# Optimization experiments

Measured on AMD Instinct MI355X. Metric: run time of the kernel, lower is better.

## Reference

```python
import jax, jax.numpy as jnp
import numpy as np


def conv1d(x, w, b, pad):
    # x: [B, C, T], w: [O, I, K], b: [O]
    y = jax.lax.conv_general_dilated(x, w, (1,), [(pad, pad)],
                                     dimension_numbers=('NCH', 'OIH', 'NCH'))
    return y + b[None, :, None]


def chan_ln(x, g, b, eps=1e-4):
    # channel LayerNorm on [B, C, T] (normalize over C)
    mu = jnp.mean(x, axis=1, keepdims=True)
    var = jnp.mean((x - mu) ** 2, axis=1, keepdims=True)
    return (x - mu) * jax.lax.rsqrt(var + eps) * g[None, :, None] + b[None, :, None]


def setup_inputs() -> dict:
    key = jax.random.key(0)
    ks = jax.random.split(key, 16)
    B, Tph, Tmel, H, W = 8, 512, 4096, 256, 256
    x = jax.random.normal(ks[0], (B, Tph, H), jnp.float32)
    x_mask = jnp.ones((B, Tph, 1), jnp.float32)
    x2word = jnp.sort(jax.random.randint(ks[1], (B, Tph), 1, W + 1), axis=1)
    mel2word = jnp.sort(jax.random.randint(ks[2], (B, Tmel), 1, W + 1), axis=1)
    s = 0.05
    pre_w1 = jax.random.normal(ks[3], (H, H, 5), jnp.float32) * s
    pre_b1 = jnp.zeros((H,), jnp.float32)
    ln1_g = jnp.ones((H,), jnp.float32)
    ln1_b = jnp.zeros((H,), jnp.float32)
    pre_w2 = jax.random.normal(ks[4], (H, H, 5), jnp.float32) * s
    pre_b2 = jnp.zeros((H,), jnp.float32)
    ln2_g = jnp.ones((H,), jnp.float32)
    ln2_b = jnp.zeros((H,), jnp.float32)
    proj_w = jax.random.normal(ks[5], (H, H, 1), jnp.float32) * s
    proj_b = jnp.zeros((H,), jnp.float32)
    gauss_w = jax.random.normal(ks[6], (2, H, 1), jnp.float32) * s
    gauss_b = jnp.zeros((2,), jnp.float32)
    return {'x': x, 'x_mask': x_mask,
            'pre_w1': pre_w1, 'pre_b1': pre_b1, 'ln1_g': ln1_g, 'ln1_b': ln1_b,
            'pre_w2': pre_w2, 'pre_b2': pre_b2, 'ln2_g': ln2_g, 'ln2_b': ln2_b,
            'proj_w': proj_w, 'proj_b': proj_b,
            'gauss_w': gauss_w, 'gauss_b': gauss_b,
            'x2word': x2word, 'mel2word': mel2word, 'word_len': 256}


def reference(x, x_mask, pre_w1, pre_b1, ln1_g, ln1_b, pre_w2, pre_b2,
              ln2_g, ln2_b, proj_w, proj_b, gauss_w, gauss_b,
              x2word, mel2word, word_len):
    res_x = x                                   # [B, Tph, H]
    xt = jnp.swapaxes(x, 1, 2)                  # [B, H, Tph]
    mt = jnp.swapaxes(x_mask, 1, 2)             # [B, 1, Tph]
    # ConvReluNorm pre-net (dropout p=0)
    h = jax.nn.relu(chan_ln(conv1d(xt * mt, pre_w1, pre_b1, 2), ln1_g, ln1_b))
    h = jax.nn.relu(chan_ln(conv1d(h * mt, pre_w2, pre_b2, 2), ln2_g, ln2_b))
    h = (xt + conv1d(h, proj_w, proj_b, 0)) * mt
    # gaussian head -> per-phone duration mean m
    g = conv1d(h, gauss_w, gauss_b, 0)          # [B, 2, Tph]
    m = (jax.nn.relu(g[:, 0:1]) + 1.0) * mt
    m = m[:, 0, :]                              # [B, Tph]
    B, Tph = x2word.shape
    Tmel = mel2word.shape[1]
    W = word_len
    bidx = jnp.arange(B)[:, None]
    # scatter-add per-phone durations into word slots (slot 0 = pad)
    dur = jnp.zeros((B, W + 1), m.dtype).at[bidx, x2word].add(m)
    m_word = dur[:, 1:]                         # [B, W]
    # mel2ph_to_dur: frame counts per word
    dur_word = jnp.zeros((B, W + 1), m.dtype).at[bidx, mel2word].add(
        jnp.ones(mel2word.shape, m.dtype))[:, 1:]
    scale = dur_word / (m_word + 1e-4)
    scale_ph = jnp.pad(scale, ((0, 0), (1, 0)))[bidx, x2word]   # gather to phones
    m = m + (scale_ph - 1.0) * jax.lax.stop_gradient(m)
    # Gaussian soft alignment
    center = jnp.cumsum(m, axis=1) - m / 2                      # [B, Tph]
    pos = jnp.arange(Tmel, dtype=m.dtype)
    diff = center[:, None, :] - pos[None, :, None]              # [B, Tmel, Tph]
    y_mask = (mel2word > 0).astype(m.dtype)[:, :, None]
    yx = (mel2word[:, :, None] == x2word[:, None, :]).astype(m.dtype)
    yx = yx * y_mask * mt                                       # [B, Tmel, Tph]
    logits = -(diff * diff) / 10.0
    masked = logits - (1.0 - yx) * 1e9
    weights = jax.nn.softmax(masked.astype(jnp.float32), axis=2)
    attn = jnp.einsum('bmp,bph->bmh', weights, res_x)           # [B, Tmel, H]
    return attn, weights, m_word
```

## Files before the change

kernel.cpp:

```cpp
#include <hip/hip_runtime.h>
#include <math.h>

#define BATCH 8
#define TPH   512
#define TMEL  4096
#define HCH   256
#define WLEN  256
#define KKTOT 1280
#define PSZ   (TMEL * HCH)
#define ZSPLIT 4

#define OFF_H1  655360
#define OFF_M   2752512
#define OFF_CEN 2756608
#define OFF_GVH 2760704

typedef __attribute__((ext_vector_type(4))) float f32x4;
typedef __attribute__((ext_vector_type(8))) short bf16x8;
typedef __attribute__((ext_vector_type(8))) ushort ushort8v;

__device__ __forceinline__ double wsum_d(double v) {
#pragma unroll
    for (int o = 32; o > 0; o >>= 1) v += __shfl_xor(v, o);
    return v;
}
__device__ __forceinline__ float wmax_f(float v) {
#pragma unroll
    for (int o = 32; o > 0; o >>= 1) v = fmaxf(v, __shfl_xor(v, o));
    return v;
}

__device__ __forceinline__ ushort f2bf(float f) {
    unsigned u = __float_as_uint(f);
    return (ushort)((u + 0x7fffu + ((u >> 16) & 1u)) >> 16);
}
__device__ __forceinline__ float bf2f(ushort h) {
    return __uint_as_float((unsigned)h << 16);
}
__device__ __forceinline__ int sidx(int row, int ch) {
    return row * 64 + (ch ^ ((row & 7) << 3));
}

__global__ __launch_bounds__(256) void k_pre(const float* __restrict__ w1,
                                             const float* __restrict__ w2,
                                             ushort* __restrict__ bh1,
                                             ushort* __restrict__ bl1,
                                             ushort* __restrict__ bh2,
                                             ushort* __restrict__ bl2,
                                             const float* __restrict__ gw,
                                             const float* __restrict__ projw,
                                             const float* __restrict__ projb,
                                             double* __restrict__ gvh) {
    __shared__ double part[4];
    int idx = blockIdx.x;
    if (idx < 512) {
        const float* src = (idx < 256) ? w1 : w2;
        ushort* dh = (idx < 256) ? bh1 : bh2;
        ushort* dl = (idx < 256) ? bl1 : bl2;
        int o = idx & 255;
        int t = threadIdx.x;
#pragma unroll
        for (int j = 0; j < 5; ++j) {
            int kk = t + j * 256;
            int k = kk >> 8, i = kk & 255;
            float v = src[o * KKTOT + i * 5 + k];
            ushort h = f2bf(v);
            dh[(size_t)o * KKTOT + kk] = h;
            dl[(size_t)o * KKTOT + kk] = f2bf(v - bf2f(h));
        }
        return;
    }
    int i = threadIdx.x;
    int lane = i & 63, wid = i >> 6;
    double a0 = 0.0, a1 = 0.0, a2 = 0.0, a3 = 0.0;
#pragma unroll 4
    for (int c = 0; c < HCH; c += 4) {
        a0 += (double)gw[c + 0] * (double)projw[(c + 0) * HCH + i];
        a1 += (double)gw[c + 1] * (double)projw[(c + 1) * HCH + i];
        a2 += (double)gw[c + 2] * (double)projw[(c + 2) * HCH + i];
        a3 += (double)gw[c + 3] * (double)projw[(c + 3) * HCH + i];
    }
    gvh[i] = ((a0 + a1) + (a2 + a3));
    double s = wsum_d((double)gw[i] * (double)projb[i]);
    if (lane == 0) part[wid] = s;
    __syncthreads();
    if (i == 0) gvh[256] = part[0] + part[1] + part[2] + part[3];
}

__device__ __forceinline__ void stage_a_row(ushort* AsH, ushort* AsL,
                                            const float* __restrict__ src,
                                            const float* __restrict__ mask,
                                            int mb0, int mrow0, int ci0,
                                            int row, int cq) {
    int rib = mrow0 - 2 + row;
    bool v = ((unsigned)rib < 512u);
    const float* sp = src + (size_t)(mb0 + (v ? rib : 0)) * HCH + ci0 + cq * 16;
    float mk = v ? mask[mb0 + rib] : 0.0f;
    float4 f0 = ((const float4*)sp)[0];
    float4 f1 = ((const float4*)sp)[1];
    float4 f2 = ((const float4*)sp)[2];
    float4 f3 = ((const float4*)sp)[3];
    float va[16] = {f0.x, f0.y, f0.z, f0.w, f1.x, f1.y, f1.z, f1.w,
                    f2.x, f2.y, f2.z, f2.w, f3.x, f3.y, f3.z, f3.w};
    ushort h[16], l[16];
#pragma unroll
    for (int j = 0; j < 16; ++j) {
        float m = va[j] * mk;
        h[j] = f2bf(m);
        l[j] = f2bf(m - bf2f(h[j]));
    }
    ushort8v hv0 = {h[0], h[1], h[2], h[3], h[4], h[5], h[6], h[7]};
    ushort8v hv1 = {h[8], h[9], h[10], h[11], h[12], h[13], h[14], h[15]};
    ushort8v lv0 = {l[0], l[1], l[2], l[3], l[4], l[5], l[6], l[7]};
    ushort8v lv1 = {l[8], l[9], l[10], l[11], l[12], l[13], l[14], l[15]};
    *(ushort8v*)&AsH[sidx(row, cq * 16 + 0)] = hv0;
    *(ushort8v*)&AsH[sidx(row, cq * 16 + 8)] = hv1;
    *(ushort8v*)&AsL[sidx(row, cq * 16 + 0)] = lv0;
    *(ushort8v*)&AsL[sidx(row, cq * 16 + 8)] = lv1;
}

__global__ __launch_bounds__(256) void k_conv_mfma(const float* __restrict__ src,
                                                   const float* __restrict__ mask,
                                                   const ushort* __restrict__ BhT,
                                                   const ushort* __restrict__ BlT,
                                                   float* __restrict__ pout) {
    __shared__ __align__(16) ushort AsH[68 * 64];
    __shared__ __align__(16) ushort AsL[68 * 64];
    __shared__ __align__(16) ushort BsH[64 * 64];
    __shared__ __align__(16) ushort BsL[64 * 64];
    int t = threadIdx.x;
    int lane = t & 63, w = t >> 6;
    int wr = w >> 1, wc = w & 1;
    int l15 = lane & 15, lk = lane >> 4;
    int c0 = blockIdx.x * 64;
    int m0 = blockIdx.y * 64;
    int ci0 = blockIdx.z * 64;
    float* out = pout + (size_t)blockIdx.z * PSZ;
    int mb0 = m0 & ~511, mrow0 = m0 & 511;

    {
        int r = t >> 2, cq = t & 3;
        stage_a_row(AsH, AsL, src, mask, mb0, mrow0, ci0, r, cq);
        if (t < 16) stage_a_row(AsH, AsL, src, mask, mb0, mrow0, ci0, 64 + (t >> 2), t & 3);
    }

    f32x4 acc00 = {0.f, 0.f, 0.f, 0.f}, acc01 = {0.f, 0.f, 0.f, 0.f};
    f32x4 acc10 = {0.f, 0.f, 0.f, 0.f}, acc11 = {0.f, 0.f, 0.f, 0.f};

    int bcol = t >> 2, bkq = t & 3;
    size_t gbase = (size_t)(c0 + bcol) * KKTOT + ci0 + bkq * 16;
    ushort8v pbh0 = *(const ushort8v*)(BhT + gbase);
    ushort8v pbh1 = *(const ushort8v*)(BhT + gbase + 8);
    ushort8v pbl0 = *(const ushort8v*)(BlT + gbase);
    ushort8v pbl1 = *(const ushort8v*)(BlT + gbase + 8);

#pragma unroll 1
    for (int k5 = 0; k5 < 5; ++k5) {
        __syncthreads();
        *(ushort8v*)&BsH[sidx(bcol, bkq * 16 + 0)] = pbh0;
        *(ushort8v*)&BsH[sidx(bcol, bkq * 16 + 8)] = pbh1;
        *(ushort8v*)&BsL[sidx(bcol, bkq * 16 + 0)] = pbl0;
        *(ushort8v*)&BsL[sidx(bcol, bkq * 16 + 8)] = pbl1;
        __syncthreads();
        if (k5 < 4) {
            size_t g2 = gbase + (size_t)(k5 + 1) * 256;
            pbh0 = *(const ushort8v*)(BhT + g2);
            pbh1 = *(const ushort8v*)(BhT + g2 + 8);
            pbl0 = *(const ushort8v*)(BlT + g2);
            pbl1 = *(const ushort8v*)(BlT + g2 + 8);
        }
#pragma unroll
        for (int kc = 0; kc < 2; ++kc) {
            int ach = kc * 32 + lk * 8;
            int ar0 = wr * 32 + l15 + k5;
            bf16x8 aH0 = *(const bf16x8*)&AsH[sidx(ar0, ach)];
            bf16x8 aH1 = *(const bf16x8*)&AsH[sidx(ar0 + 16, ach)];
            bf16x8 aL0 = *(const bf16x8*)&AsL[sidx(ar0, ach)];
            bf16x8 aL1 = *(const bf16x8*)&AsL[sidx(ar0 + 16, ach)];
            int bc0 = wc * 32 + l15;
            bf16x8 bH0 = *(const bf16x8*)&BsH[sidx(bc0, ach)];
            bf16x8 bH1 = *(const bf16x8*)&BsH[sidx(bc0 + 16, ach)];
            bf16x8 bL0 = *(const bf16x8*)&BsL[sidx(bc0, ach)];
            bf16x8 bL1 = *(const bf16x8*)&BsL[sidx(bc0 + 16, ach)];
#define MM(a, b, c) c = __builtin_amdgcn_mfma_f32_16x16x32_bf16(a, b, c, 0, 0, 0)
            MM(aH0, bH0, acc00); MM(aH0, bL0, acc00); MM(aL0, bH0, acc00);
            MM(aH0, bH1, acc01); MM(aH0, bL1, acc01); MM(aL0, bH1, acc01);
            MM(aH1, bH0, acc10); MM(aH1, bL0, acc10); MM(aL1, bH0, acc10);
            MM(aH1, bH1, acc11); MM(aH1, bL1, acc11); MM(aL1, bH1, acc11);
#undef MM
        }
    }
    int rb = m0 + wr * 32 + lk * 4;
    int cb = c0 + wc * 32 + l15;
#pragma unroll
    for (int i = 0; i < 4; ++i) {
        out[(size_t)(rb + i) * HCH + cb]           = acc00[i];
        out[(size_t)(rb + i) * HCH + cb + 16]      = acc01[i];
        out[(size_t)(rb + 16 + i) * HCH + cb]      = acc10[i];
        out[(size_t)(rb + 16 + i) * HCH + cb + 16] = acc11[i];
    }
}

__global__ __launch_bounds__(256) void k_ln_relu(const float* __restrict__ p,
                                                 const float* __restrict__ bias,
                                                 const float* __restrict__ g,
                                                 const float* __restrict__ b,
                                                 float* __restrict__ out) {
    int lane = threadIdx.x & 63, wid = threadIdx.x >> 6;
    int row = blockIdx.x * 4 + wid;
    int c4 = lane * 4;
    size_t idx = (size_t)row * HCH + c4;
    float4 bs = *(const float4*)(bias + c4);
    double s0 = bs.x, s1 = bs.y, s2 = bs.z, s3 = bs.w;
#pragma unroll
    for (int z = 0; z < ZSPLIT; z++) {
        float4 pv = *(const float4*)(p + (size_t)z * PSZ + idx);
        s0 += pv.x; s1 += pv.y; s2 += pv.z; s3 += pv.w;
    }
    double mu = wsum_d(((s0 + s1) + (s2 + s3))) * (1.0 / 256.0);
    double w0 = s0 - mu, w1 = s1 - mu, w2 = s2 - mu, w3 = s3 - mu;
    double var = wsum_d((w0 * w0 + w1 * w1) + (w2 * w2 + w3 * w3)) * (1.0 / 256.0);
    double rs = 1.0 / sqrt(var + 1e-4);
    float4 gg = *(const float4*)(g + c4);
    float4 bb = *(const float4*)(b + c4);
    float4 o;
    o.x = (float)fmax(w0 * rs * (double)gg.x + (double)bb.x, 0.0);
    o.y = (float)fmax(w1 * rs * (double)gg.y + (double)bb.y, 0.0);
    o.z = (float)fmax(w2 * rs * (double)gg.z + (double)bb.z, 0.0);
    o.w = (float)fmax(w3 * rs * (double)gg.w + (double)bb.w, 0.0);
    *(float4*)(out + idx) = o;
}

__global__ __launch_bounds__(256) void k_ln_relu_m(const float* __restrict__ p,
                                                   const float* __restrict__ bias,
                                                   const float* __restrict__ g,
                                                   const float* __restrict__ b,
                                                   const float* __restrict__ x,
                                                   const float* __restrict__ gw,
                                                   const double* __restrict__ gvh,
                                                   const float* __restrict__ gb,
                                                   const float* __restrict__ mask,
                                                   double* __restrict__ mbuf) {
    int lane = threadIdx.x & 63, wid = threadIdx.x >> 6;
    int row = blockIdx.x * 4 + wid;
    int c4 = lane * 4;
    size_t idx = (size_t)row * HCH + c4;
    float4 bs = *(const float4*)(bias + c4);
    double s0 = bs.x, s1 = bs.y, s2 = bs.z, s3 = bs.w;
#pragma unroll
    for (int z = 0; z < ZSPLIT; z++) {
        float4 pv = *(const float4*)(p + (size_t)z * PSZ + idx);
        s0 += pv.x; s1 += pv.y; s2 += pv.z; s3 += pv.w;
    }
    double mu = wsum_d(((s0 + s1) + (s2 + s3))) * (1.0 / 256.0);
    double w0 = s0 - mu, w1 = s1 - mu, w2 = s2 - mu, w3 = s3 - mu;
    double var = wsum_d((w0 * w0 + w1 * w1) + (w2 * w2 + w3 * w3)) * (1.0 / 256.0);
    double rs = 1.0 / sqrt(var + 1e-4);
    float4 gg = *(const float4*)(g + c4);
    float4 bb = *(const float4*)(b + c4);
    double o0 = fmax(w0 * rs * (double)gg.x + (double)bb.x, 0.0);
    double o1 = fmax(w1 * rs * (double)gg.y + (double)bb.y, 0.0);
    double o2 = fmax(w2 * rs * (double)gg.z + (double)bb.z, 0.0);
    double o3 = fmax(w3 * rs * (double)gg.w + (double)bb.w, 0.0);
    double2 gv0 = *(const double2*)(gvh + c4);
    double2 gv1 = *(const double2*)(gvh + c4 + 2);
    float4 xv = *(const float4*)(x + idx);
    float4 gwv = *(const float4*)(gw + c4);
    double red = gv0.x * o0 + gv0.y * o1 + gv1.x * o2 + gv1.y * o3
               + (double)gwv.x * (double)xv.x + (double)gwv.y * (double)xv.y
               + (double)gwv.z * (double)xv.z + (double)gwv.w * (double)xv.w;
    double tot = wsum_d(red);
    if (lane == 0) {
        double mk = (double)mask[row];
        double g0 = mk * (tot + gvh[256]) + (double)gb[0];
        mbuf[row] = (fmax(g0, 0.0) + 1.0) * mk;
    }
}

__global__ __launch_bounds__(512) void k_dur(const double* __restrict__ mbuf,
                                             const int* __restrict__ x2w,
                                             const int* __restrict__ m2w,
                                             double* __restrict__ center,
                                             float* __restrict__ out_mword) {
    __shared__ double ms[512];
    __shared__ int xw[512];
    __shared__ double dur[257];
    __shared__ int firstw[257];
    __shared__ int cntw[257];
    __shared__ double sa[512], sb[512];
    int b = blockIdx.x, tid = threadIdx.x;
    if (tid < 257) { cntw[tid] = 0; dur[tid] = 0.0; }
    ms[tid] = mbuf[b * TPH + tid];
    {
        int w = x2w[b * TPH + tid];
        xw[tid] = max(0, min(256, w));
    }
    __syncthreads();
    for (int j = 0; j < TMEL / 512; j++) {
        int ww = m2w[b * TMEL + tid + j * 512];
        ww = max(0, min(256, ww));
        atomicAdd(&cntw[ww], 1);
    }
    sa[tid] = ms[tid];
    __syncthreads();
    double* cur = sa; double* nxt = sb;
#pragma unroll
    for (int off = 1; off < 512; off <<= 1) {
        double v = cur[tid];
        if (tid >= off) v += cur[tid - off];
        nxt[tid] = v;
        __syncthreads();
        double* tp = cur; cur = nxt; nxt = tp;
    }
    int w = xw[tid];
    if (tid == 0 || xw[tid - 1] != w) firstw[w] = tid;
    __syncthreads();
    if (tid == 511 || xw[tid + 1] != w) {
        int f = firstw[w];
        dur[w] = cur[tid] - ((f > 0) ? cur[f - 1] : 0.0);
    }
    __syncthreads();
    if (tid >= 1 && tid <= 256) out_mword[b * WLEN + tid - 1] = (float)dur[tid];
    double msc;
    {
        double sc = (double)cntw[w] / (dur[w] + 1e-4);
        msc = ms[tid] + (sc - 1.0) * ms[tid];
    }
    __syncthreads();
    cur[tid] = msc;
    __syncthreads();
#pragma unroll
    for (int off = 1; off < 512; off <<= 1) {
        double v = cur[tid];
        if (tid >= off) v += cur[tid - off];
        nxt[tid] = v;
        __syncthreads();
        double* tp = cur; cur = nxt; nxt = tp;
    }
    center[b * TPH + tid] = cur[tid] - msc * 0.5;
}

__global__ __launch_bounds__(256) void k_attn(const float* __restrict__ x,
                                              const double* __restrict__ center,
                                              const int* __restrict__ x2w,
                                              const int* __restrict__ m2w,
                                              const float* __restrict__ mask,
                                              float* __restrict__ outA,
                                              float* __restrict__ outW) {
    int lane = threadIdx.x & 63, wid = threadIdx.x >> 6;
    int r = blockIdx.x * 4 + wid;
    int b = r >> 12;
    const double* cen = center + b * TPH + lane * 8;
    const int* xw = x2w + b * TPH + lane * 8;
    const float* mk = mask + b * TPH + lane * 8;
    int wv = m2w[r];
    float ymf = (wv > 0) ? 1.0f : 0.0f;
    double posd = (double)(r & 4095);

    double cl[8]; int xl[8]; float ml[8];
#pragma unroll
    for (int q = 0; q < 4; q++) {
        double2 cv = ((const double2*)cen)[q];
        cl[2 * q] = cv.x; cl[2 * q + 1] = cv.y;
    }
    {
        int4 x0 = ((const int4*)xw)[0], x1 = ((const int4*)xw)[1];
        xl[0] = x0.x; xl[1] = x0.y; xl[2] = x0.z; xl[3] = x0.w;
        xl[4] = x1.x; xl[5] = x1.y; xl[6] = x1.z; xl[7] = x1.w;
        float4 m0 = ((const float4*)mk)[0], m1 = ((const float4*)mk)[1];
        ml[0] = m0.x; ml[1] = m0.y; ml[2] = m0.z; ml[3] = m0.w;
        ml[4] = m1.x; ml[5] = m1.y; ml[6] = m1.z; ml[7] = m1.w;
    }

    float ev[8];
    float lmax = -3.0e38f;
#pragma unroll
    for (int j = 0; j < 8; j++) {
        float df = (float)(cl[j] - posd);
        float lg = __fdiv_rn(df * df, -10.0f);
        float f = ((xl[j] == wv) ? ymf : 0.0f) * ml[j];
        float m32 = lg - (1.0f - f) * 1.0e9f;
        ev[j] = m32;
        lmax = fmaxf(lmax, m32);
    }
    lmax = wmax_f(lmax);
    double lsum = 0.0;
#pragma unroll
    for (int j = 0; j < 8; j++) {
        float e = __expf(__fsub_rn(ev[j], lmax));
        ev[j] = e;
        lsum += (double)e;
    }
    lsum = wsum_d(lsum);
    float tot = (float)lsum;
    float* wrow = outW + (size_t)r * TPH + lane * 8;
    bool any = false;
#pragma unroll
    for (int j = 0; j < 8; j++) {
        float w = __fdiv_rn(ev[j], tot);
        ev[j] = w;
        any |= (w > 0.f);
    }
    if (any) {
        float4 w0 = {ev[0], ev[1], ev[2], ev[3]};
        float4 w1 = {ev[4], ev[5], ev[6], ev[7]};
        ((float4*)wrow)[0] = w0;
        ((float4*)wrow)[1] = w1;
    }
    double acc0 = 0.0, acc1 = 0.0, acc2 = 0.0, acc3 = 0.0;
    const float* xb = x + (size_t)b * TPH * HCH;
    unsigned long long mball = __ballot(any);
    while (mball) {
        int l2 = __ffsll(mball) - 1;
        mball &= mball - 1;
#pragma unroll
        for (int j = 0; j < 8; j++) {
            float w = __shfl(ev[j], l2);
            if (w > 0.f) {
                int t = l2 * 8 + j;
                float4 xv = ((const float4*)(xb + (size_t)t * HCH))[lane];
                acc0 += (double)w * (double)xv.x;
                acc1 += (double)w * (double)xv.y;
                acc2 += (double)w * (double)xv.z;
                acc3 += (double)w * (double)xv.w;
            }
        }
    }
    float4 o;
    o.x = (float)acc0; o.y = (float)acc1; o.z = (float)acc2; o.w = (float)acc3;
    ((float4*)(outA + (size_t)r * HCH))[lane] = o;
}

extern "C" void kernel_launch(void* const* d_in, const int* in_sizes, int n_in,
                              void* d_out, int out_size, void* d_ws, size_t ws_size,
                              hipStream_t stream) {
    (void)in_sizes; (void)n_in; (void)out_size; (void)ws_size;
    const float* x    = (const float*)d_in[0];
    const float* xm   = (const float*)d_in[1];
    const float* pw1  = (const float*)d_in[2];
    const float* pb1  = (const float*)d_in[3];
    const float* g1   = (const float*)d_in[4];
    const float* be1  = (const float*)d_in[5];
    const float* pw2  = (const float*)d_in[6];
    const float* pb2  = (const float*)d_in[7];
    const float* g2   = (const float*)d_in[8];
    const float* be2  = (const float*)d_in[9];
    const float* pjw  = (const float*)d_in[10];
    const float* pjb  = (const float*)d_in[11];
    const float* gw   = (const float*)d_in[12];
    const float* gb   = (const float*)d_in[13];
    const int*   x2w  = (const int*)d_in[14];
    const int*   m2w  = (const int*)d_in[15];

    double* ws   = (double*)d_ws;
    ushort* bh1  = (ushort*)ws;
    ushort* bl1  = bh1 + 256 * KKTOT;
    ushort* bh2  = bl1 + 256 * KKTOT;
    ushort* bl2  = bh2 + 256 * KKTOT;
    float*  h1   = (float*)(ws + OFF_H1);
    double* mbuf = ws + OFF_M;
    double* cen  = ws + OFF_CEN;
    double* gvh  = ws + OFF_GVH;

    float* outA = (float*)d_out;
    float* outW = outA + (size_t)BATCH * TMEL * HCH;
    float* outM = outW + (size_t)BATCH * TMEL * TPH;
    float* pbuf = outA;

    hipLaunchKernelGGL(k_pre, dim3(513), dim3(256), 0, stream,
                       pw1, pw2, bh1, bl1, bh2, bl2, gw, pjw, pjb, gvh);
    hipLaunchKernelGGL(k_conv_mfma, dim3(4, 64, ZSPLIT), dim3(256), 0, stream, x, xm, bh1, bl1, pbuf);
    hipLaunchKernelGGL(k_ln_relu, dim3(1024), dim3(256), 0, stream, pbuf, pb1, g1, be1, h1);
    hipLaunchKernelGGL(k_conv_mfma, dim3(4, 64, ZSPLIT), dim3(256), 0, stream, h1, xm, bh2, bl2, pbuf);
    hipLaunchKernelGGL(k_ln_relu_m, dim3(1024), dim3(256), 0, stream, pbuf, pb2, g2, be2,
                       x, gw, gvh, gb, xm, mbuf);
    hipLaunchKernelGGL(k_dur, dim3(BATCH), dim3(512), 0, stream, mbuf, x2w, m2w, cen, outM);
    hipLaunchKernelGGL(k_attn, dim3(BATCH * TMEL / 4), dim3(256), 0, stream, x, cen, x2w, m2w, xm, outA, outW);
}
```

Measured before the change: 215.6 us.

## Emit bf16 hi/lo split from LN kernel, lighten barriers, float attn accumulation

The first LN/ReLU kernel now applies the mask and writes the activation pre-split into bf16 high/low halves, so the second conv loads ready-made bf16 tiles instead of reading fp32 and converting per block (each value was converted several times across blocks). The conv barriers are replaced with an LDS-only wait plus s_barrier, avoiding a wait on outstanding global loads. The attention weighted sum accumulates in fp32 instead of fp64, which cuts double-precision FMA cost but may lose some accuracy.

```diff
diff --git a/kernel.cpp b/kernel.cpp
--- a/kernel.cpp
+++ b/kernel.cpp
@@ -28,6 +28,12 @@
 #pragma unroll
     for (int o = 32; o > 0; o >>= 1) v = fmaxf(v, __shfl_xor(v, o));
     return v;
+}
+
+__device__ __forceinline__ void bar_lds() {
+    asm volatile("s_waitcnt lgkmcnt(0)" ::: "memory");
+    __builtin_amdgcn_s_barrier();
+    asm volatile("" ::: "memory");
 }
 
 __device__ __forceinline__ ushort f2bf(float f) {
@@ -87,39 +93,55 @@
     if (i == 0) gvh[256] = part[0] + part[1] + part[2] + part[3];
 }
 
+template <int MODE>
 __device__ __forceinline__ void stage_a_row(ushort* AsH, ushort* AsL,
-                                            const float* __restrict__ src,
+                                            const float* __restrict__ srcF,
+                                            const ushort* __restrict__ srcH,
+                                            const ushort* __restrict__ srcL,
                                             const float* __restrict__ mask,
                                             int mb0, int mrow0, int ci0,
                                             int row, int cq) {
     int rib = mrow0 - 2 + row;
     bool v = ((unsigned)rib < 512u);
-    const float* sp = src + (size_t)(mb0 + (v ? rib : 0)) * HCH + ci0 + cq * 16;
-    float mk = v ? mask[mb0 + rib] : 0.0f;
-    float4 f0 = ((const float4*)sp)[0];
-    float4 f1 = ((const float4*)sp)[1];
-    float4 f2 = ((const float4*)sp)[2];
-    float4 f3 = ((const float4*)sp)[3];
-    float va[16] = {f0.x, f0.y, f0.z, f0.w, f1.x, f1.y, f1.z, f1.w,
-                    f2.x, f2.y, f2.z, f2.w, f3.x, f3.y, f3.z, f3.w};
-    ushort h[16], l[16];
-#pragma unroll
-    for (int j = 0; j < 16; ++j) {
-        float m = va[j] * mk;
-        h[j] = f2bf(m);
-        l[j] = f2bf(m - bf2f(h[j]));
-    }
-    ushort8v hv0 = {h[0], h[1], h[2], h[3], h[4], h[5], h[6], h[7]};
-    ushort8v hv1 = {h[8], h[9], h[10], h[11], h[12], h[13], h[14], h[15]};
-    ushort8v lv0 = {l[0], l[1], l[2], l[3], l[4], l[5], l[6], l[7]};
-    ushort8v lv1 = {l[8], l[9], l[10], l[11], l[12], l[13], l[14], l[15]};
+    size_t off = (size_t)(mb0 + (v ? rib : 0)) * HCH + ci0 + cq * 16;
+    ushort8v hv0, hv1, lv0, lv1;
+    if (MODE == 1) {
+        ushort8v z = {0, 0, 0, 0, 0, 0, 0, 0};
+        hv0 = v ? *(const ushort8v*)(srcH + off) : z;
+        hv1 = v ? *(const ushort8v*)(srcH + off + 8) : z;
+        lv0 = v ? *(const ushort8v*)(srcL + off) : z;
+        lv1 = v ? *(const ushort8v*)(srcL + off + 8) : z;
+    } else {
+        const float* sp = srcF + off;
+        float mk = v ? mask[mb0 + rib] : 0.0f;
+        float4 f0 = ((const float4*)sp)[0];
+        float4 f1 = ((const float4*)sp)[1];
+        float4 f2 = ((const float4*)sp)[2];
+        float4 f3 = ((const float4*)sp)[3];
+        float va[16] = {f0.x, f0.y, f0.z, f0.w, f1.x, f1.y, f1.z, f1.w,
+                        f2.x, f2.y, f2.z, f2.w, f3.x, f3.y, f3.z, f3.w};
+        ushort h[16], l[16];
+#pragma unroll
+        for (int j = 0; j < 16; ++j) {
+            float m = va[j] * mk;
+            h[j] = f2bf(m);
+            l[j] = f2bf(m - bf2f(h[j]));
+        }
+        hv0 = (ushort8v){h[0], h[1], h[2], h[3], h[4], h[5], h[6], h[7]};
+        hv1 = (ushort8v){h[8], h[9], h[10], h[11], h[12], h[13], h[14], h[15]};
+        lv0 = (ushort8v){l[0], l[1], l[2], l[3], l[4], l[5], l[6], l[7]};
+        lv1 = (ushort8v){l[8], l[9], l[10], l[11], l[12], l[13], l[14], l[15]};
+    }
     *(ushort8v*)&AsH[sidx(row, cq * 16 + 0)] = hv0;
     *(ushort8v*)&AsH[sidx(row, cq * 16 + 8)] = hv1;
     *(ushort8v*)&AsL[sidx(row, cq * 16 + 0)] = lv0;
     *(ushort8v*)&AsL[sidx(row, cq * 16 + 8)] = lv1;
 }
 
-__global__ __launch_bounds__(256) void k_conv_mfma(const float* __restrict__ src,
+template <int MODE>
+__global__ __launch_bounds__(256) void k_conv_mfma(const float* __restrict__ srcF,
+                                                   const ushort* __restrict__ srcH,
+                                                   const ushort* __restrict__ srcL,
                                                    const float* __restrict__ mask,
                                                    const ushort* __restrict__ BhT,
                                                    const ushort* __restrict__ BlT,
@@ -140,8 +162,10 @@
 
     {
         int r = t >> 2, cq = t & 3;
-        stage_a_row(AsH, AsL, src, mask, mb0, mrow0, ci0, r, cq);
-        if (t < 16) stage_a_row(AsH, AsL, src, mask, mb0, mrow0, ci0, 64 + (t >> 2), t & 3);
+        stage_a_row<MODE>(AsH, AsL, srcF, srcH, srcL, mask, mb0, mrow0, ci0, r, cq);
+        if (t < 16)
+            stage_a_row<MODE>(AsH, AsL, srcF, srcH, srcL, mask, mb0, mrow0, ci0,
+                              64 + (t >> 2), t & 3);
     }
 
     f32x4 acc00 = {0.f, 0.f, 0.f, 0.f}, acc01 = {0.f, 0.f, 0.f, 0.f};
@@ -156,12 +180,12 @@
 
 #pragma unroll 1
     for (int k5 = 0; k5 < 5; ++k5) {
-        __syncthreads();
+        bar_lds();
         *(ushort8v*)&BsH[sidx(bcol, bkq * 16 + 0)] = pbh0;
         *(ushort8v*)&BsH[sidx(bcol, bkq * 16 + 8)] = pbh1;
         *(ushort8v*)&BsL[sidx(bcol, bkq * 16 + 0)] = pbl0;
         *(ushort8v*)&BsL[sidx(bcol, bkq * 16 + 8)] = pbl1;
-        __syncthreads();
+        bar_lds();
         if (k5 < 4) {
             size_t g2 = gbase + (size_t)(k5 + 1) * 256;
             pbh0 = *(const ushort8v*)(BhT + g2);
@@ -205,7 +229,9 @@
                                                  const float* __restrict__ bias,
                                                  const float* __restrict__ g,
                                                  const float* __restrict__ b,
-                                                 float* __restrict__ out) {
+                                                 const float* __restrict__ mask,
+                                                 ushort* __restrict__ outH,
+                                                 ushort* __restrict__ outL) {
     int lane = threadIdx.x & 63, wid = threadIdx.x >> 6;
     int row = blockIdx.x * 4 + wid;
     int c4 = lane * 4;
@@ -223,12 +249,22 @@
     double rs = 1.0 / sqrt(var + 1e-4);
     float4 gg = *(const float4*)(g + c4);
     float4 bb = *(const float4*)(b + c4);
-    float4 o;
-    o.x = (float)fmax(w0 * rs * (double)gg.x + (double)bb.x, 0.0);
-    o.y = (float)fmax(w1 * rs * (double)gg.y + (double)bb.y, 0.0);
-    o.z = (float)fmax(w2 * rs * (double)gg.z + (double)bb.z, 0.0);
-    o.w = (float)fmax(w3 * rs * (double)gg.w + (double)bb.w, 0.0);
-    *(float4*)(out + idx) = o;
+    float mk = mask[row];
+    float of[4];
+    of[0] = (float)fmax(w0 * rs * (double)gg.x + (double)bb.x, 0.0) * mk;
+    of[1] = (float)fmax(w1 * rs * (double)gg.y + (double)bb.y, 0.0) * mk;
+    of[2] = (float)fmax(w2 * rs * (double)gg.z + (double)bb.z, 0.0) * mk;
+    of[3] = (float)fmax(w3 * rs * (double)gg.w + (double)bb.w, 0.0) * mk;
+    ushort4 hh, hl;
+    ushort* hp = (ushort*)&hh; ushort* lp = (ushort*)&hl;
+#pragma unroll
+    for (int j = 0; j < 4; ++j) {
+        ushort h = f2bf(of[j]);
+        hp[j] = h;
+        lp[j] = f2bf(of[j] - bf2f(h));
+    }
+    *(ushort4*)(outH + idx) = hh;
+    *(ushort4*)(outL + idx) = hl;
 }
 
 __global__ __launch_bounds__(256) void k_ln_relu_m(const float* __restrict__ p,
@@ -407,7 +443,7 @@
         ((float4*)wrow)[0] = w0;
         ((float4*)wrow)[1] = w1;
     }
-    double acc0 = 0.0, acc1 = 0.0, acc2 = 0.0, acc3 = 0.0;
+    float acc0 = 0.f, acc1 = 0.f, acc2 = 0.f, acc3 = 0.f;
     const float* xb = x + (size_t)b * TPH * HCH;
     unsigned long long mball = __ballot(any);
     while (mball) {
@@ -419,15 +455,15 @@
             if (w > 0.f) {
                 int t = l2 * 8 + j;
                 float4 xv = ((const float4*)(xb + (size_t)t * HCH))[lane];
-                acc0 += (double)w * (double)xv.x;
-                acc1 += (double)w * (double)xv.y;
-                acc2 += (double)w * (double)xv.z;
-                acc3 += (double)w * (double)xv.w;
+                acc0 += w * xv.x;
+                acc1 += w * xv.y;
+                acc2 += w * xv.z;
+                acc3 += w * xv.w;
             }
         }
     }
     float4 o;
-    o.x = (float)acc0; o.y = (float)acc1; o.z = (float)acc2; o.w = (float)acc3;
+    o.x = acc0; o.y = acc1; o.z = acc2; o.w = acc3;
     ((float4*)(outA + (size_t)r * HCH))[lane] = o;
 }
 
@@ -457,7 +493,8 @@
     ushort* bl1  = bh1 + 256 * KKTOT;
     ushort* bh2  = bl1 + 256 * KKTOT;
     ushort* bl2  = bh2 + 256 * KKTOT;
-    float*  h1   = (float*)(ws + OFF_H1);
+    ushort* h1h  = (ushort*)(ws + OFF_H1);
+    ushort* h1l  = h1h + (size_t)TMEL * HCH;
     double* mbuf = ws + OFF_M;
     double* cen  = ws + OFF_CEN;
     double* gvh  = ws + OFF_GVH;
@@ -469,9 +506,12 @@
 
     hipLaunchKernelGGL(k_pre, dim3(513), dim3(256), 0, stream,
                        pw1, pw2, bh1, bl1, bh2, bl2, gw, pjw, pjb, gvh);
-    hipLaunchKernelGGL(k_conv_mfma, dim3(4, 64, ZSPLIT), dim3(256), 0, stream, x, xm, bh1, bl1, pbuf);
-    hipLaunchKernelGGL(k_ln_relu, dim3(1024), dim3(256), 0, stream, pbuf, pb1, g1, be1, h1);
-    hipLaunchKernelGGL(k_conv_mfma, dim3(4, 64, ZSPLIT), dim3(256), 0, stream, h1, xm, bh2, bl2, pbuf);
+    hipLaunchKernelGGL(k_conv_mfma<0>, dim3(4, 64, ZSPLIT), dim3(256), 0, stream,
+                       x, (const ushort*)nullptr, (const ushort*)nullptr, xm, bh1, bl1, pbuf);
+    hipLaunchKernelGGL(k_ln_relu, dim3(1024), dim3(256), 0, stream,
+                       pbuf, pb1, g1, be1, xm, h1h, h1l);
+    hipLaunchKernelGGL(k_conv_mfma<1>, dim3(4, 64, ZSPLIT), dim3(256), 0, stream,
+                       (const float*)nullptr, h1h, h1l, xm, bh2, bl2, pbuf);
     hipLaunchKernelGGL(k_ln_relu_m, dim3(1024), dim3(256), 0, stream, pbuf, pb2, g2, be2,
                        x, gw, gvh, gb, xm, mbuf);
     hipLaunchKernelGGL(k_dur, dim3(BATCH), dim3(512), 0, stream, mbuf, x2w, m2w, cen, outM);
```

Result: no change. 217.8 us (+1.0%).
